# Kernel tuning notes

Hardware: AMD Instinct MI355X
Metric: run time of the kernel (lower is better)

Reference implementation:

```python
import math
import jax, jax.numpy as jnp
import numpy as np

MAX_LEN = 2048
D_HEAD = 64
B, H, S = 4, 16, 1024


def setup_inputs() -> dict:
    key = jax.random.key(0)
    kq, kk, kp = jax.random.split(key, 3)
    q = jax.random.normal(kq, (B, H, S, D_HEAD), dtype=jnp.float32)
    k = jax.random.normal(kk, (B, H, S, D_HEAD), dtype=jnp.float32)
    pos_table = jax.random.normal(kp, (MAX_LEN, D_HEAD), dtype=jnp.float32)
    return {"q": q, "k": k, "pos_table": pos_table}


def reference(q, k, pos_table):
    d_head = q.shape[-1]
    seq_len = q.shape[2]
    max_len = pos_table.shape[0]
    scale = 1.0 / math.sqrt(d_head)
    # attention gates: (b,h,s,s)
    gates = jax.nn.sigmoid(jnp.einsum('bhsd,bhtd->bhst', q, k) * scale)
    # context positions: weighted sum of key indices -> (b,h,s)
    positions = jnp.arange(seq_len, dtype=q.dtype)
    ctx_pos = jnp.einsum('bhst,t->bhs', gates, positions)
    ctx_pos = jnp.clip(ctx_pos, 0.0, float(max_len - 2))
    pos_floor = ctx_pos.astype(jnp.int32)  # (b,h,s)
    pos_frac = (ctx_pos - pos_floor.astype(q.dtype))[..., None]  # (b,h,s,1)
    emb_floor = pos_table[pos_floor]  # (b,h,s,d)
    emb_ceil = pos_table[jnp.minimum(pos_floor + 1, max_len - 1)]
    pos_emb = emb_floor + pos_frac * (emb_ceil - emb_floor)  # (b,h,s,d)
    # bias: (b,h,s,s)
    bias = jnp.einsum('bhsd,bhtd->bhst', q, pos_emb)
    return bias
```

## Files before the change

### kernel.cpp

```cpp
#include <hip/hip_runtime.h>

#define Bb_ 4
#define Hh_ 16
#define Ss_ 1024
#define DH 64
#define MAXLEN 2048
#define BH (Bb_*Hh_)
#define LDST 72

typedef __attribute__((ext_vector_type(8))) short short8;
typedef __attribute__((ext_vector_type(4))) float floatx4;
typedef __attribute__((ext_vector_type(4))) unsigned short ushort4v;

static __device__ __forceinline__ unsigned short f2bf(float f) {
    unsigned int u = __builtin_bit_cast(unsigned int, f);
    u = (u + 0x7fffu + ((u >> 16) & 1u)) >> 16;
    return (unsigned short)u;
}

static __device__ __forceinline__ void stage_tile(unsigned short* lds,
                                                  const float* __restrict__ g,
                                                  int tid) {
#pragma unroll
    for (int it = 0; it < 8; ++it) {
        int idx = it * 1024 + tid * 4;
        int row = idx >> 6, col = idx & 63;
        const float4 v = *reinterpret_cast<const float4*>(g + row * 64 + col);
        ushort4v o = { f2bf(v.x), f2bf(v.y), f2bf(v.z), f2bf(v.w) };
        *reinterpret_cast<ushort4v*>(lds + row * LDST + col) = o;
    }
}

__global__ __launch_bounds__(256, 2)
void ctx_emb_kernel(const float* __restrict__ q, const float* __restrict__ k,
                    const float* __restrict__ tb,
                    unsigned short* __restrict__ pemb) {
    __shared__ __align__(16) unsigned short Ab[128 * LDST];
    __shared__ __align__(16) unsigned short Kb[128 * LDST];
    __shared__ float sh_ctx[128];

    int bx = blockIdx.x;
    int bh = bx >> 3, mt = bx & 7;
    int m0 = mt << 7;
    int tid = threadIdx.x;
    int lane = tid & 63, w = tid >> 6;
    int lo = lane & 15, quad = lane >> 4;

    stage_tile(Ab, q + (size_t)(bh * Ss_ + m0) * DH, tid);
    __syncthreads();

    short8 afr[2][2];
#pragma unroll
    for (int i = 0; i < 2; ++i)
#pragma unroll
        for (int k2 = 0; k2 < 2; ++k2)
            afr[i][k2] = *reinterpret_cast<const short8*>(
                &Ab[(w * 32 + i * 16 + lo) * LDST + k2 * 32 + quad * 8]);

    float rp[2][4];
#pragma unroll
    for (int i = 0; i < 2; ++i)
#pragma unroll
        for (int r = 0; r < 4; ++r) rp[i][r] = 0.f;

    for (int tt = 0; tt < 8; ++tt) {
        int t0 = tt << 7;
        __syncthreads();
        stage_tile(Kb, k + (size_t)(bh * Ss_ + t0) * DH, tid);
        __syncthreads();

#pragma unroll
        for (int j = 0; j < 8; ++j) {
            short8 b0 = *reinterpret_cast<const short8*>(
                &Kb[(j * 16 + lo) * LDST + 0 + quad * 8]);
            short8 b1 = *reinterpret_cast<const short8*>(
                &Kb[(j * 16 + lo) * LDST + 32 + quad * 8]);
            float tcol = (float)(t0 + j * 16 + lo);
#pragma unroll
            for (int i = 0; i < 2; ++i) {
                floatx4 c = {0.f, 0.f, 0.f, 0.f};
                c = __builtin_amdgcn_mfma_f32_16x16x32_bf16(afr[i][0], b0, c, 0, 0, 0);
                c = __builtin_amdgcn_mfma_f32_16x16x32_bf16(afr[i][1], b1, c, 0, 0, 0);
#pragma unroll
                for (int r = 0; r < 4; ++r) {
                    float x = c[r] * 0.125f;
                    float e = __expf(-x);
                    float g = __builtin_amdgcn_rcpf(1.0f + e);
                    rp[i][r] += g * tcol;
                }
            }
        }
    }

#pragma unroll
    for (int i = 0; i < 2; ++i)
#pragma unroll
        for (int r = 0; r < 4; ++r) {
            float v = rp[i][r];
            v += __shfl_xor(v, 1);
            v += __shfl_xor(v, 2);
            v += __shfl_xor(v, 4);
            v += __shfl_xor(v, 8);
            rp[i][r] = v;
        }

    if (lo == 0) {
#pragma unroll
        for (int i = 0; i < 2; ++i)
#pragma unroll
            for (int r = 0; r < 4; ++r) {
                int row = w * 32 + i * 16 + quad * 4 + r;
                sh_ctx[row] = fminf(fmaxf(rp[i][r], 0.f), (float)(MAXLEN - 2));
            }
    }
    __syncthreads();

    {
        int rsub = tid >> 4;
        int d0 = (tid & 15) * 4;
#pragma unroll
        for (int pass = 0; pass < 8; ++pass) {
            int row = pass * 16 + rsub;
            float c = sh_ctx[row];
            int fl = (int)c;
            float fr = c - (float)fl;
            int ce = min(fl + 1, MAXLEN - 1);
            const float4 e0 = *reinterpret_cast<const float4*>(tb + fl * DH + d0);
            const float4 e1 = *reinterpret_cast<const float4*>(tb + ce * DH + d0);
            ushort4v o = { f2bf(e0.x + fr * (e1.x - e0.x)),
                           f2bf(e0.y + fr * (e1.y - e0.y)),
                           f2bf(e0.z + fr * (e1.z - e0.z)),
                           f2bf(e0.w + fr * (e1.w - e0.w)) };
            *reinterpret_cast<ushort4v*>(
                pemb + (size_t)(bh * Ss_ + m0 + row) * DH + d0) = o;
        }
    }
}

__global__ __launch_bounds__(256, 2)
void bias_kernel(const float* __restrict__ q,
                 const unsigned short* __restrict__ pemb,
                 float* __restrict__ out) {
    __shared__ __align__(16) unsigned short Ab[128 * LDST];

    int bx = blockIdx.x;
    int bh = bx >> 3, mt = bx & 7;
    int m0 = mt << 7;
    int tid = threadIdx.x;
    int lane = tid & 63, w = tid >> 6;
    int lo = lane & 15, quad = lane >> 4;

    stage_tile(Ab, q + (size_t)(bh * Ss_ + m0) * DH, tid);
    __syncthreads();

    short8 afr[2][2];
#pragma unroll
    for (int i = 0; i < 2; ++i)
#pragma unroll
        for (int k2 = 0; k2 < 2; ++k2)
            afr[i][k2] = *reinterpret_cast<const short8*>(
                &Ab[(w * 32 + i * 16 + lo) * LDST + k2 * 32 + quad * 8]);

    const unsigned short* pb = pemb + (size_t)bh * Ss_ * DH;
    float* outb = out + (size_t)(bh * Ss_ + m0) * Ss_;

#pragma unroll 1
    for (int nt = 0; nt < 8; ++nt) {
        int n0 = nt << 7;

        floatx4 acc[2][8];
#pragma unroll
        for (int i = 0; i < 2; ++i)
#pragma unroll
            for (int j = 0; j < 8; ++j) acc[i][j] = (floatx4){0.f, 0.f, 0.f, 0.f};

#pragma unroll
        for (int j = 0; j < 8; ++j) {
            const unsigned short* bp = pb + (n0 + j * 16 + lo) * DH + quad * 8;
            short8 b0 = *reinterpret_cast<const short8*>(bp);
            short8 b1 = *reinterpret_cast<const short8*>(bp + 32);
#pragma unroll
            for (int i = 0; i < 2; ++i) {
                acc[i][j] = __builtin_amdgcn_mfma_f32_16x16x32_bf16(afr[i][0], b0, acc[i][j], 0, 0, 0);
                acc[i][j] = __builtin_amdgcn_mfma_f32_16x16x32_bf16(afr[i][1], b1, acc[i][j], 0, 0, 0);
            }
        }

#pragma unroll
        for (int i = 0; i < 2; ++i)
#pragma unroll
            for (int j = 0; j < 8; ++j)
#pragma unroll
                for (int r = 0; r < 4; ++r) {
                    int row = w * 32 + i * 16 + quad * 4 + r;
                    int col = n0 + j * 16 + lo;
                    __builtin_nontemporal_store(
                        acc[i][j][r], outb + (size_t)row * Ss_ + col);
                }
    }
}

extern "C" void kernel_launch(void* const* d_in, const int* in_sizes, int n_in,
                              void* d_out, int out_size, void* d_ws, size_t ws_size,
                              hipStream_t stream) {
    const float* q  = (const float*)d_in[0];
    const float* k  = (const float*)d_in[1];
    const float* tb = (const float*)d_in[2];
    unsigned short* pemb = (unsigned short*)d_ws;
    float* out = (float*)d_out;

    ctx_emb_kernel<<<BH * 8, 256, 0, stream>>>(q, k, tb, pemb);
    bias_kernel<<<BH * 8, 256, 0, stream>>>(q, pemb, out);
}
```

Measured before the change: 354.5 us.

## Split bias kernel over output column tiles and load Q fragments directly

The bias kernel now launches one block per (bh, row tile, column tile) instead of looping over eight column tiles inside a block, which multiplies the grid eightfold. Q fragments are loaded straight from global memory and converted to bf16 in registers, so the LDS staging and its barrier are gone. The aim is more parallelism and better latency hiding on the store-bound output write. The cost is that Q is re-read and re-converted eight times across blocks.

```diff
diff --git a/kernel.cpp b/kernel.cpp
--- a/kernel.cpp
+++ b/kernel.cpp
@@ -141,63 +141,64 @@
 void bias_kernel(const float* __restrict__ q,
                  const unsigned short* __restrict__ pemb,
                  float* __restrict__ out) {
-    __shared__ __align__(16) unsigned short Ab[128 * LDST];
-
     int bx = blockIdx.x;
-    int bh = bx >> 3, mt = bx & 7;
-    int m0 = mt << 7;
+    int nt = bx >> 9;
+    int rest = bx & 511;
+    int bh = rest >> 3, mt = rest & 7;
+    int m0 = mt << 7, n0 = nt << 7;
     int tid = threadIdx.x;
     int lane = tid & 63, w = tid >> 6;
     int lo = lane & 15, quad = lane >> 4;
 
-    stage_tile(Ab, q + (size_t)(bh * Ss_ + m0) * DH, tid);
-    __syncthreads();
-
+    const float* qb = q + (size_t)(bh * Ss_ + m0) * DH;
     short8 afr[2][2];
 #pragma unroll
     for (int i = 0; i < 2; ++i)
 #pragma unroll
-        for (int k2 = 0; k2 < 2; ++k2)
-            afr[i][k2] = *reinterpret_cast<const short8*>(
-                &Ab[(w * 32 + i * 16 + lo) * LDST + k2 * 32 + quad * 8]);
-
-    const unsigned short* pb = pemb + (size_t)bh * Ss_ * DH;
-    float* outb = out + (size_t)(bh * Ss_ + m0) * Ss_;
-
-#pragma unroll 1
-    for (int nt = 0; nt < 8; ++nt) {
-        int n0 = nt << 7;
-
-        floatx4 acc[2][8];
-#pragma unroll
-        for (int i = 0; i < 2; ++i)
-#pragma unroll
-            for (int j = 0; j < 8; ++j) acc[i][j] = (floatx4){0.f, 0.f, 0.f, 0.f};
-
-#pragma unroll
-        for (int j = 0; j < 8; ++j) {
-            const unsigned short* bp = pb + (n0 + j * 16 + lo) * DH + quad * 8;
-            short8 b0 = *reinterpret_cast<const short8*>(bp);
-            short8 b1 = *reinterpret_cast<const short8*>(bp + 32);
-#pragma unroll
-            for (int i = 0; i < 2; ++i) {
-                acc[i][j] = __builtin_amdgcn_mfma_f32_16x16x32_bf16(afr[i][0], b0, acc[i][j], 0, 0, 0);
-                acc[i][j] = __builtin_amdgcn_mfma_f32_16x16x32_bf16(afr[i][1], b1, acc[i][j], 0, 0, 0);
+        for (int k2 = 0; k2 < 2; ++k2) {
+            const float* ap = qb + (w * 32 + i * 16 + lo) * DH + k2 * 32 + quad * 8;
+            const float4 a0 = *reinterpret_cast<const float4*>(ap);
+            const float4 a1 = *reinterpret_cast<const float4*>(ap + 4);
+            short8 f;
+            f[0] = (short)f2bf(a0.x); f[1] = (short)f2bf(a0.y);
+            f[2] = (short)f2bf(a0.z); f[3] = (short)f2bf(a0.w);
+            f[4] = (short)f2bf(a1.x); f[5] = (short)f2bf(a1.y);
+            f[6] = (short)f2bf(a1.z); f[7] = (short)f2bf(a1.w);
+            afr[i][k2] = f;
+        }
+
+    const unsigned short* pb = pemb + (size_t)(bh * Ss_ + n0) * DH;
+
+    floatx4 acc[2][8];
+#pragma unroll
+    for (int i = 0; i < 2; ++i)
+#pragma unroll
+        for (int j = 0; j < 8; ++j) acc[i][j] = (floatx4){0.f, 0.f, 0.f, 0.f};
+
+#pragma unroll
+    for (int j = 0; j < 8; ++j) {
+        const unsigned short* bp = pb + (j * 16 + lo) * DH + quad * 8;
+        short8 b0 = *reinterpret_cast<const short8*>(bp);
+        short8 b1 = *reinterpret_cast<const short8*>(bp + 32);
+#pragma unroll
+        for (int i = 0; i < 2; ++i) {
+            acc[i][j] = __builtin_amdgcn_mfma_f32_16x16x32_bf16(afr[i][0], b0, acc[i][j], 0, 0, 0);
+            acc[i][j] = __builtin_amdgcn_mfma_f32_16x16x32_bf16(afr[i][1], b1, acc[i][j], 0, 0, 0);
+        }
+    }
+
+    float* outb = out + (size_t)(bh * Ss_ + m0) * Ss_ + n0;
+#pragma unroll
+    for (int i = 0; i < 2; ++i)
+#pragma unroll
+        for (int j = 0; j < 8; ++j)
+#pragma unroll
+            for (int r = 0; r < 4; ++r) {
+                int row = w * 32 + i * 16 + quad * 4 + r;
+                int col = j * 16 + lo;
+                __builtin_nontemporal_store(
+                    acc[i][j][r], outb + (size_t)row * Ss_ + col);
             }
-        }
-
-#pragma unroll
-        for (int i = 0; i < 2; ++i)
-#pragma unroll
-            for (int j = 0; j < 8; ++j)
-#pragma unroll
-                for (int r = 0; r < 4; ++r) {
-                    int row = w * 32 + i * 16 + quad * 4 + r;
-                    int col = n0 + j * 16 + lo;
-                    __builtin_nontemporal_store(
-                        acc[i][j][r], outb + (size_t)row * Ss_ + col);
-                }
-    }
 }
 
 extern "C" void kernel_launch(void* const* d_in, const int* in_sizes, int n_in,
@@ -210,5 +211,5 @@
     float* out = (float*)d_out;
 
     ctx_emb_kernel<<<BH * 8, 256, 0, stream>>>(q, k, tb, pemb);
-    bias_kernel<<<BH * 8, 256, 0, stream>>>(q, pemb, out);
-}
+    bias_kernel<<<BH * 64, 256, 0, stream>>>(q, pemb, out);
+}
```

Result: slower. 384.3 us (+8.4%).
